# Performance work log

Measured on AMD Instinct MI355X. Metric: run time of the kernel, lower is better.

## Reference

```python
import jax, jax.numpy as jnp
import numpy as np

B, L, D = 2, 1024, 2048
E, K = 8, 2
H, HS = 1408, 2816


def setup_inputs() -> dict:
    key = jax.random.key(0)
    ks = jax.random.split(key, 9)
    s = 0.02  # param init scale
    return {
        "x": jax.random.normal(ks[0], (B, L, D), dtype=jnp.float32),
        "gate_w": jax.random.normal(ks[1], (E, D), dtype=jnp.float32) * s,
        "w_gate": jax.random.normal(ks[2], (E, D, H), dtype=jnp.float32) * s,
        "w_up": jax.random.normal(ks[3], (E, D, H), dtype=jnp.float32) * s,
        "w_down": jax.random.normal(ks[4], (E, H, D), dtype=jnp.float32) * s,
        "shgate_w": jax.random.normal(ks[5], (D,), dtype=jnp.float32) * s,
        "shw_gate": jax.random.normal(ks[6], (D, HS), dtype=jnp.float32) * s,
        "shw_up": jax.random.normal(ks[7], (D, HS), dtype=jnp.float32) * s,
        "shw_down": jax.random.normal(ks[8], (HS, D), dtype=jnp.float32) * s,
    }


def reference(x, gate_w, w_gate, w_up, w_down, shgate_w, shw_gate, shw_up, shw_down):
    b, l, d = x.shape
    xf = x.reshape(-1, d)  # [T, D]

    # --- router: softmax over expert logits, top-k, renormalize ---
    logits = jnp.einsum("td,ed->te", xf.astype(jnp.float32), gate_w)
    probs = jax.nn.softmax(logits.astype(jnp.float32), axis=-1)  # [T, E]
    weights, indices = jax.lax.top_k(probs, K)                   # [T, K]
    weights = (weights / weights.sum(-1, keepdims=True)).astype(x.dtype)

    # per-token combine weight for each expert: sum of top-k weights routed to e
    onehot = jax.nn.one_hot(indices, E, dtype=x.dtype)           # [T, K, E]
    combine = jnp.einsum("tk,tke->te", weights, onehot)          # [T, E]

    # --- experts (dense vectorized equivalent of masked gather/scatter loop) ---
    g = jnp.einsum("td,edh->teh", xf, w_gate)
    u = jnp.einsum("td,edh->teh", xf, w_up)
    h = jax.nn.silu(g) * u                                       # [T, E, H]
    # fused down-proj + weighted combine; accumulate in fp32 like the original
    out = jnp.einsum("teh,ehd,te->td", h.astype(jnp.float32),
                     w_down.astype(jnp.float32), combine.astype(jnp.float32))

    # --- shared expert with sigmoid gate ---
    sgate = jax.nn.sigmoid(xf @ shgate_w)[:, None]               # [T, 1]
    sh = (jax.nn.silu(xf @ shw_gate) * (xf @ shw_up)) @ shw_down  # [T, D]
    out = out + (sgate * sh).astype(jnp.float32)

    return out.astype(x.dtype).reshape(b, l, d)
```

## Files before the change

kernel.cpp:

```cpp
#include <hip/hip_runtime.h>
#include <hip/hip_bf16.h>
#include <math.h>

#define T_TOK 2048
#define Dd    2048
#define Ee    8
#define Hh    1408
#define HSs   2816
#define CAP   1024

typedef __attribute__((ext_vector_type(8))) __bf16 bf16x8;
typedef __attribute__((ext_vector_type(4))) __bf16 bf16x4;
typedef __attribute__((ext_vector_type(4))) float  f32x4;

#define MFMA(a, b, c) __builtin_amdgcn_mfma_f32_16x16x32_bf16(a, b, c, 0, 0, 0)

__device__ __forceinline__ void async_copy16(const __bf16* g, __bf16* l) {
    __builtin_amdgcn_global_load_lds(
        (const __attribute__((address_space(1))) unsigned int*)g,
        (__attribute__((address_space(3))) unsigned int*)l, 16, 0, 0);
}

__global__ void init_cnt(int* __restrict__ cnt) {
    if (threadIdx.x < Ee) cnt[threadIdx.x] = 0;
}

__global__ __launch_bounds__(256) void router_kernel(
    const float* __restrict__ x, const float* __restrict__ gate_w,
    const float* __restrict__ shgate_w,
    int* __restrict__ cnt, int* __restrict__ ptok,
    float* __restrict__ pw, float* __restrict__ sgate)
{
    const int t = blockIdx.x;
    const int tid = threadIdx.x;
    const float* xt = x + (size_t)t * Dd;

    float acc[Ee];
#pragma unroll
    for (int e = 0; e < Ee; e++) acc[e] = 0.f;
    float accs = 0.f;

    for (int d = tid; d < Dd; d += 256) {
        float xv = xt[d];
#pragma unroll
        for (int e = 0; e < Ee; e++) acc[e] += xv * gate_w[e * Dd + d];
        accs += xv * shgate_w[d];
    }

    __shared__ float red[Ee + 1][256];
#pragma unroll
    for (int e = 0; e < Ee; e++) red[e][tid] = acc[e];
    red[Ee][tid] = accs;
    __syncthreads();

    for (int s = 128; s > 0; s >>= 1) {
        if (tid < s) {
#pragma unroll
            for (int e = 0; e <= Ee; e++) red[e][tid] += red[e][tid + s];
        }
        __syncthreads();
    }

    if (tid == 0) {
        float l0 = -1e30f, l1 = -1e30f;
        int i0 = 0, i1 = 0;
#pragma unroll
        for (int e = 0; e < Ee; e++) {
            float v = red[e][0];
            if (v > l0) { l1 = l0; i1 = i0; l0 = v; i0 = e; }
            else if (v > l1) { l1 = v; i1 = e; }
        }
        float w0 = 1.f / (1.f + expf(l1 - l0));
        float w1 = 1.f - w0;

        int p0 = atomicAdd(&cnt[i0], 1);
        if (p0 < CAP) { ptok[i0 * CAP + p0] = t; pw[i0 * CAP + p0] = w0; }
        int p1 = atomicAdd(&cnt[i1], 1);
        if (p1 < CAP) { ptok[i1 * CAP + p1] = t; pw[i1 * CAP + p1] = w1; }

        sgate[t] = 1.f / (1.f + expf(-red[Ee][0]));
    }
}

__global__ __launch_bounds__(256) void cvt_x(const float* __restrict__ src,
                                             __bf16* __restrict__ dst)
{
    int i = blockIdx.x * 256 + threadIdx.x;
    float4 v = ((const float4*)src)[i];
    bf16x4 o = { (__bf16)v.x, (__bf16)v.y, (__bf16)v.z, (__bf16)v.w };
    ((bf16x4*)dst)[i] = o;
}

__global__ __launch_bounds__(256) void transpose_cvt(
    const float* __restrict__ src, __bf16* __restrict__ dst, int R, int C)
{
    const size_t bstride = (size_t)R * C;
    src += blockIdx.z * bstride;
    dst += blockIdx.z * bstride;
    __shared__ float tile[32][33];
    const int tx = threadIdx.x, ty = threadIdx.y;
    const int c0 = blockIdx.x * 32, r0 = blockIdx.y * 32;
#pragma unroll
    for (int j = 0; j < 4; j++)
        tile[ty + 8 * j][tx] = src[(size_t)(r0 + ty + 8 * j) * C + c0 + tx];
    __syncthreads();
#pragma unroll
    for (int j = 0; j < 4; j++)
        dst[(size_t)(c0 + ty + 8 * j) * R + r0 + tx] = (__bf16)tile[tx][ty + 8 * j];
}

__global__ __launch_bounds__(256, 3) void gateup_expert(
    const __bf16* __restrict__ xb,
    const __bf16* __restrict__ wgT, const __bf16* __restrict__ wuT,
    const int* __restrict__ cnt, const int* __restrict__ ptok,
    __bf16* __restrict__ hq)
{
    const int e = blockIdx.x >> 3, mt = blockIdx.x & 7;
    int n = cnt[e]; if (n > CAP) n = CAP;
    const int m0 = mt * 128;
    if (m0 >= n) return;
    const int h0 = blockIdx.y * 64;
    const int tid = threadIdx.x, lane = tid & 63, wave = tid >> 6;

    __shared__ __align__(16) __bf16 As[128 * 32];
    __shared__ __align__(16) __bf16 Bgs[64 * 32];
    __shared__ __align__(16) __bf16 Bus[64 * 32];
    __shared__ int tok_s[128];

    if (tid < 128) {
        int i = m0 + tid; int ic = i < n ? i : n - 1;
        tok_s[tid] = ptok[e * CAP + ic];
    }
    __syncthreads();

    const int kq = (tid & 3) * 8;
    const int r1 = tid >> 2, r2 = 64 + (tid >> 2);
    const __bf16* ga1 = xb + (size_t)tok_s[r1] * Dd + kq;
    const __bf16* ga2 = xb + (size_t)tok_s[r2] * Dd + kq;
    const size_t wbase = (size_t)e * Hh * Dd + (size_t)(h0 + (tid >> 2)) * Dd + kq;
    const __bf16* gbg = wgT + wbase;
    const __bf16* gbu = wuT + wbase;
    __bf16* la1 = As + tid * 8; __bf16* la2 = As + (tid + 256) * 8;
    __bf16* lbg = Bgs + tid * 8; __bf16* lbu = Bus + tid * 8;

    f32x4 accg[2][4] = {}, accu[2][4] = {};
    const int q = lane >> 4, m = lane & 15;

    for (int k0 = 0; k0 < Dd; k0 += 32) {
        async_copy16(ga1 + k0, la1);
        async_copy16(ga2 + k0, la2);
        async_copy16(gbg + k0, lbg);
        async_copy16(gbu + k0, lbu);
        __syncthreads();
        bf16x8 af[2], bgf[4], buf_[4];
        af[0] = *(const bf16x8*)(As + (wave * 32 + m) * 32 + q * 8);
        af[1] = *(const bf16x8*)(As + (wave * 32 + 16 + m) * 32 + q * 8);
#pragma unroll
        for (int j = 0; j < 4; j++) {
            bgf[j]  = *(const bf16x8*)(Bgs + (j * 16 + m) * 32 + q * 8);
            buf_[j] = *(const bf16x8*)(Bus + (j * 16 + m) * 32 + q * 8);
        }
#pragma unroll
        for (int i = 0; i < 2; i++)
#pragma unroll
            for (int j = 0; j < 4; j++) {
                accg[i][j] = MFMA(af[i], bgf[j], accg[i][j]);
                accu[i][j] = MFMA(af[i], buf_[j], accu[i][j]);
            }
        __syncthreads();
    }

#pragma unroll
    for (int i = 0; i < 2; i++)
#pragma unroll
        for (int r = 0; r < 4; r++) {
            int row = wave * 32 + i * 16 + q * 4 + r;
            size_t p = (size_t)(e * CAP + m0 + row);
#pragma unroll
            for (int j = 0; j < 4; j++) {
                int h = h0 + j * 16 + m;
                float g = accg[i][j][r], u = accu[i][j][r];
                float s = g / (1.f + __expf(-g));
                hq[p * Hh + h] = (__bf16)(s * u);
            }
        }
}

__global__ __launch_bounds__(256, 3) void gateup_shared(
    const __bf16* __restrict__ xb,
    const __bf16* __restrict__ wgT, const __bf16* __restrict__ wuT,
    __bf16* __restrict__ shh)
{
    const int m0 = blockIdx.x * 128;
    const int h0 = blockIdx.y * 64;
    const int tid = threadIdx.x, lane = tid & 63, wave = tid >> 6;

    __shared__ __align__(16) __bf16 As[128 * 32];
    __shared__ __align__(16) __bf16 Bgs[64 * 32];
    __shared__ __align__(16) __bf16 Bus[64 * 32];

    const int kq = (tid & 3) * 8;
    const __bf16* ga1 = xb + (size_t)(m0 + (tid >> 2)) * Dd + kq;
    const __bf16* ga2 = xb + (size_t)(m0 + 64 + (tid >> 2)) * Dd + kq;
    const size_t wbase = (size_t)(h0 + (tid >> 2)) * Dd + kq;
    const __bf16* gbg = wgT + wbase;
    const __bf16* gbu = wuT + wbase;
    __bf16* la1 = As + tid * 8; __bf16* la2 = As + (tid + 256) * 8;
    __bf16* lbg = Bgs + tid * 8; __bf16* lbu = Bus + tid * 8;

    f32x4 accg[2][4] = {}, accu[2][4] = {};
    const int q = lane >> 4, m = lane & 15;

    for (int k0 = 0; k0 < Dd; k0 += 32) {
        async_copy16(ga1 + k0, la1);
        async_copy16(ga2 + k0, la2);
        async_copy16(gbg + k0, lbg);
        async_copy16(gbu + k0, lbu);
        __syncthreads();
        bf16x8 af[2], bgf[4], buf_[4];
        af[0] = *(const bf16x8*)(As + (wave * 32 + m) * 32 + q * 8);
        af[1] = *(const bf16x8*)(As + (wave * 32 + 16 + m) * 32 + q * 8);
#pragma unroll
        for (int j = 0; j < 4; j++) {
            bgf[j]  = *(const bf16x8*)(Bgs + (j * 16 + m) * 32 + q * 8);
            buf_[j] = *(const bf16x8*)(Bus + (j * 16 + m) * 32 + q * 8);
        }
#pragma unroll
        for (int i = 0; i < 2; i++)
#pragma unroll
            for (int j = 0; j < 4; j++) {
                accg[i][j] = MFMA(af[i], bgf[j], accg[i][j]);
                accu[i][j] = MFMA(af[i], buf_[j], accu[i][j]);
            }
        __syncthreads();
    }

#pragma unroll
    for (int i = 0; i < 2; i++)
#pragma unroll
        for (int r = 0; r < 4; r++) {
            int row = wave * 32 + i * 16 + q * 4 + r;
#pragma unroll
            for (int j = 0; j < 4; j++) {
                int h = h0 + j * 16 + m;
                float g = accg[i][j][r], u = accu[i][j][r];
                float s = g / (1.f + __expf(-g));
                shh[(size_t)(m0 + row) * HSs + h] = (__bf16)(s * u);
            }
        }
}

__global__ __launch_bounds__(256, 3) void down_shared(
    const __bf16* __restrict__ A,
    const __bf16* __restrict__ BT,
    const float* __restrict__ sgate,
    float* __restrict__ out)
{
    const int m0 = blockIdx.x * 128, n0 = blockIdx.y * 128;
    const int tid = threadIdx.x, lane = tid & 63, wave = tid >> 6;
    const int wr = wave >> 1, wc = wave & 1;

    __shared__ __align__(16) __bf16 As[128 * 32];
    __shared__ __align__(16) __bf16 Bs[128 * 32];

    const int kq = (tid & 3) * 8;
    const __bf16* ga1 = A + (size_t)(m0 + (tid >> 2)) * HSs + kq;
    const __bf16* ga2 = A + (size_t)(m0 + 64 + (tid >> 2)) * HSs + kq;
    const __bf16* gb1 = BT + (size_t)(n0 + (tid >> 2)) * HSs + kq;
    const __bf16* gb2 = BT + (size_t)(n0 + 64 + (tid >> 2)) * HSs + kq;
    __bf16* la1 = As + tid * 8; __bf16* la2 = As + (tid + 256) * 8;
    __bf16* lb1 = Bs + tid * 8; __bf16* lb2 = Bs + (tid + 256) * 8;

    f32x4 acc[4][4] = {};
    const int q = lane >> 4, m = lane & 15;

    for (int k0 = 0; k0 < HSs; k0 += 32) {
        async_copy16(ga1 + k0, la1);
        async_copy16(ga2 + k0, la2);
        async_copy16(gb1 + k0, lb1);
        async_copy16(gb2 + k0, lb2);
        __syncthreads();
        bf16x8 af[4], bf[4];
#pragma unroll
        for (int i = 0; i < 4; i++) {
            af[i] = *(const bf16x8*)(As + (wr * 64 + i * 16 + m) * 32 + q * 8);
            bf[i] = *(const bf16x8*)(Bs + (wc * 64 + i * 16 + m) * 32 + q * 8);
        }
#pragma unroll
        for (int i = 0; i < 4; i++)
#pragma unroll
            for (int j = 0; j < 4; j++)
                acc[i][j] = MFMA(af[i], bf[j], acc[i][j]);
        __syncthreads();
    }

#pragma unroll
    for (int i = 0; i < 4; i++)
#pragma unroll
        for (int r = 0; r < 4; r++) {
            int t = m0 + wr * 64 + i * 16 + q * 4 + r;
            float sg = sgate[t];
#pragma unroll
            for (int j = 0; j < 4; j++) {
                int d = n0 + wc * 64 + j * 16 + m;
                out[(size_t)t * Dd + d] = sg * acc[i][j][r];
            }
        }
}

__global__ __launch_bounds__(256, 3) void down_expert(
    const __bf16* __restrict__ hq,
    const __bf16* __restrict__ wdT,
    const int* __restrict__ cnt, const int* __restrict__ ptok,
    const float* __restrict__ pw,
    float* __restrict__ out)
{
    const int e = blockIdx.x >> 3, mt = blockIdx.x & 7;
    int n = cnt[e]; if (n > CAP) n = CAP;
    const int m0 = mt * 128;
    if (m0 >= n) return;
    const int n0 = blockIdx.y * 128;
    const int tid = threadIdx.x, lane = tid & 63, wave = tid >> 6;
    const int wr = wave >> 1, wc = wave & 1;

    __shared__ __align__(16) __bf16 As[128 * 32];
    __shared__ __align__(16) __bf16 Bs[128 * 32];
    __shared__ int   tok_s[128];
    __shared__ float w_s[128];

    if (tid < 128) {
        int i = m0 + tid; int ic = i < n ? i : n - 1;
        tok_s[tid] = ptok[e * CAP + ic];
        w_s[tid] = (i < n) ? pw[e * CAP + ic] : 0.f;
    }

    const int kq = (tid & 3) * 8;
    int i1 = m0 + (tid >> 2);       if (i1 > n - 1) i1 = n - 1;
    int i2 = m0 + 64 + (tid >> 2);  if (i2 > n - 1) i2 = n - 1;
    const __bf16* ga1 = hq + (size_t)(e * CAP + i1) * Hh + kq;
    const __bf16* ga2 = hq + (size_t)(e * CAP + i2) * Hh + kq;
    const __bf16* gb1 = wdT + ((size_t)e * Dd + n0 + (tid >> 2)) * Hh + kq;
    const __bf16* gb2 = wdT + ((size_t)e * Dd + n0 + 64 + (tid >> 2)) * Hh + kq;
    __bf16* la1 = As + tid * 8; __bf16* la2 = As + (tid + 256) * 8;
    __bf16* lb1 = Bs + tid * 8; __bf16* lb2 = Bs + (tid + 256) * 8;

    f32x4 acc[4][4] = {};
    const int q = lane >> 4, m = lane & 15;

    for (int k0 = 0; k0 < Hh; k0 += 32) {
        async_copy16(ga1 + k0, la1);
        async_copy16(ga2 + k0, la2);
        async_copy16(gb1 + k0, lb1);
        async_copy16(gb2 + k0, lb2);
        __syncthreads();
        bf16x8 af[4], bf[4];
#pragma unroll
        for (int i = 0; i < 4; i++) {
            af[i] = *(const bf16x8*)(As + (wr * 64 + i * 16 + m) * 32 + q * 8);
            bf[i] = *(const bf16x8*)(Bs + (wc * 64 + i * 16 + m) * 32 + q * 8);
        }
#pragma unroll
        for (int i = 0; i < 4; i++)
#pragma unroll
            for (int j = 0; j < 4; j++)
                acc[i][j] = MFMA(af[i], bf[j], acc[i][j]);
        __syncthreads();
    }

#pragma unroll
    for (int i = 0; i < 4; i++)
#pragma unroll
        for (int r = 0; r < 4; r++) {
            int row = wr * 64 + i * 16 + q * 4 + r;
            if (m0 + row < n) {
                int   tok = tok_s[row];
                float w   = w_s[row];
#pragma unroll
                for (int j = 0; j < 4; j++) {
                    int d = n0 + wc * 64 + j * 16 + m;
                    atomicAdd(&out[(size_t)tok * Dd + d], w * acc[i][j][r]);
                }
            }
        }
}

extern "C" void kernel_launch(void* const* d_in, const int* in_sizes, int n_in,
                              void* d_out, int out_size, void* d_ws, size_t ws_size,
                              hipStream_t stream) {
    const float* x        = (const float*)d_in[0];
    const float* gate_w   = (const float*)d_in[1];
    const float* w_gate   = (const float*)d_in[2];
    const float* w_up     = (const float*)d_in[3];
    const float* w_down   = (const float*)d_in[4];
    const float* shgate_w = (const float*)d_in[5];
    const float* shw_gate = (const float*)d_in[6];
    const float* shw_up   = (const float*)d_in[7];
    const float* shw_down = (const float*)d_in[8];
    float* out = (float*)d_out;

    char* ws = (char*)d_ws;
    size_t off = 0;
    auto alloc = [&](size_t bytes) { char* p = ws + off; off = (off + bytes + 255) & ~(size_t)255; return p; };
    int*    cnt    = (int*)   alloc(Ee * 4);
    int*    ptok   = (int*)   alloc(Ee * CAP * 4);
    float*  pw     = (float*) alloc(Ee * CAP * 4);
    float*  sgate  = (float*) alloc(T_TOK * 4);
    __bf16* xb     = (__bf16*)alloc((size_t)T_TOK * Dd * 2);
    __bf16* wgT    = (__bf16*)alloc((size_t)Ee * Hh * Dd * 2);
    __bf16* wuT    = (__bf16*)alloc((size_t)Ee * Hh * Dd * 2);
    __bf16* wdT    = (__bf16*)alloc((size_t)Ee * Dd * Hh * 2);
    __bf16* shwgT  = (__bf16*)alloc((size_t)HSs * Dd * 2);
    __bf16* shwuT  = (__bf16*)alloc((size_t)HSs * Dd * 2);
    __bf16* shwdT  = (__bf16*)alloc((size_t)Dd * HSs * 2);
    __bf16* hq     = (__bf16*)alloc((size_t)Ee * CAP * Hh * 2);
    __bf16* shh    = (__bf16*)alloc((size_t)T_TOK * HSs * 2);

    dim3 b256(256), bT(32, 8);

    init_cnt<<<dim3(1), dim3(64), 0, stream>>>(cnt);
    cvt_x<<<dim3(T_TOK * Dd / 4 / 256), b256, 0, stream>>>(x, xb);
    transpose_cvt<<<dim3(Hh / 32, Dd / 32, Ee), bT, 0, stream>>>(w_gate, wgT, Dd, Hh);
    transpose_cvt<<<dim3(Hh / 32, Dd / 32, Ee), bT, 0, stream>>>(w_up, wuT, Dd, Hh);
    transpose_cvt<<<dim3(Dd / 32, Hh / 32, Ee), bT, 0, stream>>>(w_down, wdT, Hh, Dd);
    transpose_cvt<<<dim3(HSs / 32, Dd / 32, 1), bT, 0, stream>>>(shw_gate, shwgT, Dd, HSs);
    transpose_cvt<<<dim3(HSs / 32, Dd / 32, 1), bT, 0, stream>>>(shw_up, shwuT, Dd, HSs);
    transpose_cvt<<<dim3(Dd / 32, HSs / 32, 1), bT, 0, stream>>>(shw_down, shwdT, HSs, Dd);

    router_kernel<<<dim3(T_TOK), b256, 0, stream>>>(x, gate_w, shgate_w, cnt, ptok, pw, sgate);

    gateup_expert<<<dim3(Ee * 8, Hh / 64), b256, 0, stream>>>(xb, wgT, wuT, cnt, ptok, hq);
    gateup_shared<<<dim3(T_TOK / 128, HSs / 64), b256, 0, stream>>>(xb, shwgT, shwuT, shh);
    down_shared<<<dim3(T_TOK / 128, Dd / 128), b256, 0, stream>>>(shh, shwdT, sgate, out);
    down_expert<<<dim3(Ee * 8, Dd / 128), b256, 0, stream>>>(hq, wdT, cnt, ptok, pw, out);
}
```

Baseline: 763.2 us.

## Merge expert and shared GEMMs into single launches, replace atomics with slot combine

Expert and shared-expert gate/up GEMMs now run in one kernel, and both down-projection GEMMs run in another. This cuts launches and lets the two workloads fill the GPU together. Expert outputs go to a per-token slot buffer instead of float atomicAdd into the output, and a separate combine kernel sums the slots. The LDS staging is laid out per-wave to match the MFMA fragment layout, and the weight transpose uses 64x64 tiles with paired bf16 stores. The cost is an extra 32MB fp32 intermediate plus a combine pass over it. Gate/up tiles are also split across waves, exchanging the up accumulators through LDS.

```diff
diff --git a/kernel.cpp b/kernel.cpp
--- a/kernel.cpp
+++ b/kernel.cpp
@@ -11,6 +11,7 @@
 
 typedef __attribute__((ext_vector_type(8))) __bf16 bf16x8;
 typedef __attribute__((ext_vector_type(4))) __bf16 bf16x4;
+typedef __attribute__((ext_vector_type(2))) __bf16 bf16x2;
 typedef __attribute__((ext_vector_type(4))) float  f32x4;
 
 #define MFMA(a, b, c) __builtin_amdgcn_mfma_f32_16x16x32_bf16(a, b, c, 0, 0, 0)
@@ -28,7 +29,7 @@
 __global__ __launch_bounds__(256) void router_kernel(
     const float* __restrict__ x, const float* __restrict__ gate_w,
     const float* __restrict__ shgate_w,
-    int* __restrict__ cnt, int* __restrict__ ptok,
+    int* __restrict__ cnt, int* __restrict__ ptok, int* __restrict__ pslot,
     float* __restrict__ pw, float* __restrict__ sgate)
 {
     const int t = blockIdx.x;
@@ -74,10 +75,15 @@
         float w1 = 1.f - w0;
 
         int p0 = atomicAdd(&cnt[i0], 1);
-        if (p0 < CAP) { ptok[i0 * CAP + p0] = t; pw[i0 * CAP + p0] = w0; }
+        if (p0 < CAP) {
+            ptok[i0 * CAP + p0] = t; pslot[i0 * CAP + p0] = 2 * t;
+            pw[i0 * CAP + p0] = w0;
+        }
         int p1 = atomicAdd(&cnt[i1], 1);
-        if (p1 < CAP) { ptok[i1 * CAP + p1] = t; pw[i1 * CAP + p1] = w1; }
-
+        if (p1 < CAP) {
+            ptok[i1 * CAP + p1] = t; pslot[i1 * CAP + p1] = 2 * t + 1;
+            pw[i1 * CAP + p1] = w1;
+        }
         sgate[t] = 1.f / (1.f + expf(-red[Ee][0]));
     }
 }
@@ -94,276 +100,208 @@
 __global__ __launch_bounds__(256) void transpose_cvt(
     const float* __restrict__ src, __bf16* __restrict__ dst, int R, int C)
 {
-    const size_t bstride = (size_t)R * C;
-    src += blockIdx.z * bstride;
-    dst += blockIdx.z * bstride;
-    __shared__ float tile[32][33];
-    const int tx = threadIdx.x, ty = threadIdx.y;
-    const int c0 = blockIdx.x * 32, r0 = blockIdx.y * 32;
-#pragma unroll
-    for (int j = 0; j < 4; j++)
-        tile[ty + 8 * j][tx] = src[(size_t)(r0 + ty + 8 * j) * C + c0 + tx];
+    src += (size_t)blockIdx.z * R * C;
+    dst += (size_t)blockIdx.z * R * C;
+    __shared__ float tile[64][65];
+    const int tid = threadIdx.x, tx = tid & 63, ty = tid >> 6;
+    const int c0 = blockIdx.x * 64, r0 = blockIdx.y * 64;
+#pragma unroll
+    for (int j = 0; j < 16; j++) {
+        int r = j * 4 + ty;
+        tile[r][tx] = src[(size_t)(r0 + r) * C + c0 + tx];
+    }
     __syncthreads();
-#pragma unroll
-    for (int j = 0; j < 4; j++)
-        dst[(size_t)(c0 + ty + 8 * j) * R + r0 + tx] = (__bf16)tile[tx][ty + 8 * j];
-}
-
-__global__ __launch_bounds__(256, 3) void gateup_expert(
+    const int rp = (tid & 31) * 2;
+    const int cg = tid >> 5;
+#pragma unroll
+    for (int j = 0; j < 8; j++) {
+        int c = j * 8 + cg;
+        bf16x2 v = { (__bf16)tile[rp][c], (__bf16)tile[rp + 1][c] };
+        *(bf16x2*)&dst[(size_t)(c0 + c) * R + r0 + rp] = v;
+    }
+}
+
+__global__ __launch_bounds__(256, 3) void gateup_all(
     const __bf16* __restrict__ xb,
     const __bf16* __restrict__ wgT, const __bf16* __restrict__ wuT,
+    const __bf16* __restrict__ shwgT, const __bf16* __restrict__ shwuT,
     const int* __restrict__ cnt, const int* __restrict__ ptok,
-    __bf16* __restrict__ hq)
-{
-    const int e = blockIdx.x >> 3, mt = blockIdx.x & 7;
-    int n = cnt[e]; if (n > CAP) n = CAP;
-    const int m0 = mt * 128;
-    if (m0 >= n) return;
-    const int h0 = blockIdx.y * 64;
-    const int tid = threadIdx.x, lane = tid & 63, wave = tid >> 6;
-
-    __shared__ __align__(16) __bf16 As[128 * 32];
-    __shared__ __align__(16) __bf16 Bgs[64 * 32];
-    __shared__ __align__(16) __bf16 Bus[64 * 32];
-    __shared__ int tok_s[128];
-
-    if (tid < 128) {
-        int i = m0 + tid; int ic = i < n ? i : n - 1;
-        tok_s[tid] = ptok[e * CAP + ic];
-    }
-    __syncthreads();
-
-    const int kq = (tid & 3) * 8;
-    const int r1 = tid >> 2, r2 = 64 + (tid >> 2);
-    const __bf16* ga1 = xb + (size_t)tok_s[r1] * Dd + kq;
-    const __bf16* ga2 = xb + (size_t)tok_s[r2] * Dd + kq;
-    const size_t wbase = (size_t)e * Hh * Dd + (size_t)(h0 + (tid >> 2)) * Dd + kq;
-    const __bf16* gbg = wgT + wbase;
-    const __bf16* gbu = wuT + wbase;
-    __bf16* la1 = As + tid * 8; __bf16* la2 = As + (tid + 256) * 8;
-    __bf16* lbg = Bgs + tid * 8; __bf16* lbu = Bus + tid * 8;
-
-    f32x4 accg[2][4] = {}, accu[2][4] = {};
-    const int q = lane >> 4, m = lane & 15;
-
-    for (int k0 = 0; k0 < Dd; k0 += 32) {
-        async_copy16(ga1 + k0, la1);
-        async_copy16(ga2 + k0, la2);
-        async_copy16(gbg + k0, lbg);
-        async_copy16(gbu + k0, lbu);
-        __syncthreads();
-        bf16x8 af[2], bgf[4], buf_[4];
-        af[0] = *(const bf16x8*)(As + (wave * 32 + m) * 32 + q * 8);
-        af[1] = *(const bf16x8*)(As + (wave * 32 + 16 + m) * 32 + q * 8);
-#pragma unroll
-        for (int j = 0; j < 4; j++) {
-            bgf[j]  = *(const bf16x8*)(Bgs + (j * 16 + m) * 32 + q * 8);
-            buf_[j] = *(const bf16x8*)(Bus + (j * 16 + m) * 32 + q * 8);
-        }
-#pragma unroll
-        for (int i = 0; i < 2; i++)
-#pragma unroll
-            for (int j = 0; j < 4; j++) {
-                accg[i][j] = MFMA(af[i], bgf[j], accg[i][j]);
-                accu[i][j] = MFMA(af[i], buf_[j], accu[i][j]);
-            }
-        __syncthreads();
-    }
-
-#pragma unroll
-    for (int i = 0; i < 2; i++)
-#pragma unroll
-        for (int r = 0; r < 4; r++) {
-            int row = wave * 32 + i * 16 + q * 4 + r;
-            size_t p = (size_t)(e * CAP + m0 + row);
-#pragma unroll
-            for (int j = 0; j < 4; j++) {
-                int h = h0 + j * 16 + m;
-                float g = accg[i][j][r], u = accu[i][j][r];
-                float s = g / (1.f + __expf(-g));
-                hq[p * Hh + h] = (__bf16)(s * u);
-            }
-        }
-}
-
-__global__ __launch_bounds__(256, 3) void gateup_shared(
-    const __bf16* __restrict__ xb,
-    const __bf16* __restrict__ wgT, const __bf16* __restrict__ wuT,
-    __bf16* __restrict__ shh)
-{
-    const int m0 = blockIdx.x * 128;
-    const int h0 = blockIdx.y * 64;
-    const int tid = threadIdx.x, lane = tid & 63, wave = tid >> 6;
-
-    __shared__ __align__(16) __bf16 As[128 * 32];
-    __shared__ __align__(16) __bf16 Bgs[64 * 32];
-    __shared__ __align__(16) __bf16 Bus[64 * 32];
-
-    const int kq = (tid & 3) * 8;
-    const __bf16* ga1 = xb + (size_t)(m0 + (tid >> 2)) * Dd + kq;
-    const __bf16* ga2 = xb + (size_t)(m0 + 64 + (tid >> 2)) * Dd + kq;
-    const size_t wbase = (size_t)(h0 + (tid >> 2)) * Dd + kq;
-    const __bf16* gbg = wgT + wbase;
-    const __bf16* gbu = wuT + wbase;
-    __bf16* la1 = As + tid * 8; __bf16* la2 = As + (tid + 256) * 8;
-    __bf16* lbg = Bgs + tid * 8; __bf16* lbu = Bus + tid * 8;
-
-    f32x4 accg[2][4] = {}, accu[2][4] = {};
-    const int q = lane >> 4, m = lane & 15;
-
-    for (int k0 = 0; k0 < Dd; k0 += 32) {
-        async_copy16(ga1 + k0, la1);
-        async_copy16(ga2 + k0, la2);
-        async_copy16(gbg + k0, lbg);
-        async_copy16(gbu + k0, lbu);
-        __syncthreads();
-        bf16x8 af[2], bgf[4], buf_[4];
-        af[0] = *(const bf16x8*)(As + (wave * 32 + m) * 32 + q * 8);
-        af[1] = *(const bf16x8*)(As + (wave * 32 + 16 + m) * 32 + q * 8);
-#pragma unroll
-        for (int j = 0; j < 4; j++) {
-            bgf[j]  = *(const bf16x8*)(Bgs + (j * 16 + m) * 32 + q * 8);
-            buf_[j] = *(const bf16x8*)(Bus + (j * 16 + m) * 32 + q * 8);
-        }
-#pragma unroll
-        for (int i = 0; i < 2; i++)
-#pragma unroll
-            for (int j = 0; j < 4; j++) {
-                accg[i][j] = MFMA(af[i], bgf[j], accg[i][j]);
-                accu[i][j] = MFMA(af[i], buf_[j], accu[i][j]);
-            }
-        __syncthreads();
-    }
-
-#pragma unroll
-    for (int i = 0; i < 2; i++)
-#pragma unroll
-        for (int r = 0; r < 4; r++) {
-            int row = wave * 32 + i * 16 + q * 4 + r;
-#pragma unroll
-            for (int j = 0; j < 4; j++) {
-                int h = h0 + j * 16 + m;
-                float g = accg[i][j][r], u = accu[i][j][r];
-                float s = g / (1.f + __expf(-g));
-                shh[(size_t)(m0 + row) * HSs + h] = (__bf16)(s * u);
-            }
-        }
-}
-
-__global__ __launch_bounds__(256, 3) void down_shared(
-    const __bf16* __restrict__ A,
-    const __bf16* __restrict__ BT,
-    const float* __restrict__ sgate,
-    float* __restrict__ out)
-{
-    const int m0 = blockIdx.x * 128, n0 = blockIdx.y * 128;
+    __bf16* __restrict__ hq, __bf16* __restrict__ shh)
+{
+    const int bx = blockIdx.x;
     const int tid = threadIdx.x, lane = tid & 63, wave = tid >> 6;
     const int wr = wave >> 1, wc = wave & 1;
-
-    __shared__ __align__(16) __bf16 As[128 * 32];
-    __shared__ __align__(16) __bf16 Bs[128 * 32];
-
-    const int kq = (tid & 3) * 8;
-    const __bf16* ga1 = A + (size_t)(m0 + (tid >> 2)) * HSs + kq;
-    const __bf16* ga2 = A + (size_t)(m0 + 64 + (tid >> 2)) * HSs + kq;
-    const __bf16* gb1 = BT + (size_t)(n0 + (tid >> 2)) * HSs + kq;
-    const __bf16* gb2 = BT + (size_t)(n0 + 64 + (tid >> 2)) * HSs + kq;
-    __bf16* la1 = As + tid * 8; __bf16* la2 = As + (tid + 256) * 8;
-    __bf16* lb1 = Bs + tid * 8; __bf16* lb2 = Bs + (tid + 256) * 8;
+    const int lm = lane & 15, lq = lane >> 4;
+
+    bool sh;
+    int m0, h0, n, e = 0;
+    const __bf16 *bg_mat, *bu_mat;
+    if (bx < 1408) {
+        sh = false;
+        int mtg = bx / 22, ht = bx - mtg * 22;
+        e = mtg >> 3; m0 = (mtg & 7) * 128; h0 = ht * 64;
+        n = cnt[e]; if (n > CAP) n = CAP;
+        if (m0 >= n) return;
+        bg_mat = wgT + (size_t)e * Hh * Dd;
+        bu_mat = wuT + (size_t)e * Hh * Dd;
+    } else {
+        sh = true;
+        int s = bx - 1408;
+        int mt = s / 44, ht = s - mt * 44;
+        m0 = mt * 128; h0 = ht * 64; n = T_TOK;
+        bg_mat = shwgT; bu_mat = shwuT;
+    }
+
+    __shared__ __align__(16) __bf16 stage[8192];
+    __shared__ int tok_s[128];
+
+    if (tid < 128) {
+        int i = m0 + tid;
+        if (sh) tok_s[tid] = i;
+        else { int ic = i < n ? i : n - 1; tok_s[tid] = ptok[e * CAP + ic]; }
+    }
+    __syncthreads();
+
+    const __bf16* pa0 = xb + (size_t)tok_s[wave * 16 + lm] * Dd + lq * 8;
+    const __bf16* pa1 = xb + (size_t)tok_s[64 + wave * 16 + lm] * Dd + lq * 8;
+    const __bf16* pbg = bg_mat + (size_t)(h0 + wave * 16 + lm) * Dd + lq * 8;
+    const __bf16* pbu = bu_mat + (size_t)(h0 + wave * 16 + lm) * Dd + lq * 8;
+    __bf16* la0 = stage + wave * 512 + lane * 8;
+    __bf16* la1 = stage + (4 + wave) * 512 + lane * 8;
+    __bf16* lbg = stage + 4096 + wave * 512 + lane * 8;
+    __bf16* lbu = stage + 6144 + wave * 512 + lane * 8;
 
     f32x4 acc[4][4] = {};
-    const int q = lane >> 4, m = lane & 15;
-
-    for (int k0 = 0; k0 < HSs; k0 += 32) {
-        async_copy16(ga1 + k0, la1);
-        async_copy16(ga2 + k0, la2);
-        async_copy16(gb1 + k0, lb1);
-        async_copy16(gb2 + k0, lb2);
-        __syncthreads();
-        bf16x8 af[4], bf[4];
-#pragma unroll
-        for (int i = 0; i < 4; i++) {
-            af[i] = *(const bf16x8*)(As + (wr * 64 + i * 16 + m) * 32 + q * 8);
-            bf[i] = *(const bf16x8*)(Bs + (wc * 64 + i * 16 + m) * 32 + q * 8);
-        }
+
+    for (int k0 = 0; k0 < Dd; k0 += 32) {
+        async_copy16(pa0, la0); async_copy16(pa1, la1);
+        async_copy16(pbg, lbg); async_copy16(pbu, lbu);
+        pa0 += 32; pa1 += 32; pbg += 32; pbu += 32;
+        __syncthreads();
+        bf16x8 af[4], bfr[4];
+        const __bf16* bbase = stage + (wc ? 6144 : 4096);
+#pragma unroll
+        for (int i = 0; i < 4; i++)
+            af[i] = *(const bf16x8*)(stage + (wr * 4 + i) * 512 + lane * 8);
+#pragma unroll
+        for (int j = 0; j < 4; j++)
+            bfr[j] = *(const bf16x8*)(bbase + j * 512 + lane * 8);
 #pragma unroll
         for (int i = 0; i < 4; i++)
 #pragma unroll
             for (int j = 0; j < 4; j++)
-                acc[i][j] = MFMA(af[i], bf[j], acc[i][j]);
-        __syncthreads();
-    }
-
-#pragma unroll
-    for (int i = 0; i < 4; i++)
-#pragma unroll
-        for (int r = 0; r < 4; r++) {
-            int t = m0 + wr * 64 + i * 16 + q * 4 + r;
-            float sg = sgate[t];
+                acc[i][j] = MFMA(af[i], bfr[j], acc[i][j]);
+        __syncthreads();
+    }
+
+    if (wc == 1) {
+#pragma unroll
+        for (int i = 0; i < 4; i++)
 #pragma unroll
             for (int j = 0; j < 4; j++) {
-                int d = n0 + wc * 64 + j * 16 + m;
-                out[(size_t)t * Dd + d] = sg * acc[i][j][r];
+                bf16x4 uv;
+#pragma unroll
+                for (int r = 0; r < 4; r++) uv[r] = (__bf16)acc[i][j][r];
+                *(bf16x4*)(stage + ((wr * 4 + i) * 4 + j) * 256 + lane * 4) = uv;
             }
-        }
-}
-
-__global__ __launch_bounds__(256, 3) void down_expert(
-    const __bf16* __restrict__ hq,
-    const __bf16* __restrict__ wdT,
-    const int* __restrict__ cnt, const int* __restrict__ ptok,
-    const float* __restrict__ pw,
-    float* __restrict__ out)
-{
-    const int e = blockIdx.x >> 3, mt = blockIdx.x & 7;
-    int n = cnt[e]; if (n > CAP) n = CAP;
-    const int m0 = mt * 128;
-    if (m0 >= n) return;
-    const int n0 = blockIdx.y * 128;
+    }
+    __syncthreads();
+    if (wc == 0) {
+#pragma unroll
+        for (int i = 0; i < 4; i++)
+#pragma unroll
+            for (int j = 0; j < 4; j++) {
+                bf16x4 uv = *(const bf16x4*)(stage + ((wr * 4 + i) * 4 + j) * 256 + lane * 4);
+                int col = h0 + j * 16 + lm;
+#pragma unroll
+                for (int r = 0; r < 4; r++) {
+                    int grow = m0 + wr * 64 + i * 16 + lq * 4 + r;
+                    if (!sh && grow >= n) continue;
+                    float g = acc[i][j][r], u = (float)uv[r];
+                    float hv = g / (1.f + __expf(-g)) * u;
+                    if (sh) shh[(size_t)grow * HSs + col] = (__bf16)hv;
+                    else    hq[((size_t)e * CAP + grow) * Hh + col] = (__bf16)hv;
+                }
+            }
+    }
+}
+
+__global__ __launch_bounds__(256, 3) void down_all(
+    const __bf16* __restrict__ hq, const __bf16* __restrict__ wdT,
+    const __bf16* __restrict__ shh, const __bf16* __restrict__ shwdT,
+    const int* __restrict__ cnt, const int* __restrict__ pslot,
+    const float* __restrict__ pw, const float* __restrict__ sgate,
+    float* __restrict__ eo, float* __restrict__ out)
+{
+    const int bx = blockIdx.x;
     const int tid = threadIdx.x, lane = tid & 63, wave = tid >> 6;
     const int wr = wave >> 1, wc = wave & 1;
-
-    __shared__ __align__(16) __bf16 As[128 * 32];
-    __shared__ __align__(16) __bf16 Bs[128 * 32];
-    __shared__ int   tok_s[128];
+    const int lm = lane & 15, lq = lane >> 4;
+
+    bool sh;
+    int m0, n0, n, e = 0, kdim;
+    if (bx < 1024) {
+        sh = false;
+        e = bx >> 7; m0 = ((bx >> 4) & 7) * 128; n0 = (bx & 15) * 128;
+        n = cnt[e]; if (n > CAP) n = CAP;
+        if (m0 >= n) return;
+        kdim = Hh;
+    } else {
+        sh = true;
+        int s = bx - 1024;
+        m0 = (s >> 4) * 128; n0 = (s & 15) * 128; n = T_TOK;
+        kdim = HSs;
+    }
+
+    __shared__ __align__(16) __bf16 stage[8192];
+    __shared__ int   slot_s[128];
     __shared__ float w_s[128];
 
-    if (tid < 128) {
+    if (!sh && tid < 128) {
         int i = m0 + tid; int ic = i < n ? i : n - 1;
-        tok_s[tid] = ptok[e * CAP + ic];
+        slot_s[tid] = pslot[e * CAP + ic];
         w_s[tid] = (i < n) ? pw[e * CAP + ic] : 0.f;
     }
 
-    const int kq = (tid & 3) * 8;
-    int i1 = m0 + (tid >> 2);       if (i1 > n - 1) i1 = n - 1;
-    int i2 = m0 + 64 + (tid >> 2);  if (i2 > n - 1) i2 = n - 1;
-    const __bf16* ga1 = hq + (size_t)(e * CAP + i1) * Hh + kq;
-    const __bf16* ga2 = hq + (size_t)(e * CAP + i2) * Hh + kq;
-    const __bf16* gb1 = wdT + ((size_t)e * Dd + n0 + (tid >> 2)) * Hh + kq;
-    const __bf16* gb2 = wdT + ((size_t)e * Dd + n0 + 64 + (tid >> 2)) * Hh + kq;
-    __bf16* la1 = As + tid * 8; __bf16* la2 = As + (tid + 256) * 8;
-    __bf16* lb1 = Bs + tid * 8; __bf16* lb2 = Bs + (tid + 256) * 8;
+    int ar0 = m0 + wave * 16 + lm, ar1 = m0 + 64 + wave * 16 + lm;
+    const __bf16 *pa0, *pa1, *pb0, *pb1;
+    if (sh) {
+        pa0 = shh + (size_t)ar0 * HSs + lq * 8;
+        pa1 = shh + (size_t)ar1 * HSs + lq * 8;
+        pb0 = shwdT + (size_t)(n0 + wave * 16 + lm) * HSs + lq * 8;
+        pb1 = shwdT + (size_t)(n0 + 64 + wave * 16 + lm) * HSs + lq * 8;
+    } else {
+        int a0c = ar0 < n ? ar0 : n - 1;
+        int a1c = ar1 < n ? ar1 : n - 1;
+        pa0 = hq + ((size_t)e * CAP + a0c) * Hh + lq * 8;
+        pa1 = hq + ((size_t)e * CAP + a1c) * Hh + lq * 8;
+        pb0 = wdT + ((size_t)e * Dd + n0 + wave * 16 + lm) * Hh + lq * 8;
+        pb1 = wdT + ((size_t)e * Dd + n0 + 64 + wave * 16 + lm) * Hh + lq * 8;
+    }
+    __bf16* la0 = stage + wave * 512 + lane * 8;
+    __bf16* la1 = stage + (4 + wave) * 512 + lane * 8;
+    __bf16* lb0 = stage + 4096 + wave * 512 + lane * 8;
+    __bf16* lb1 = stage + 4096 + (4 + wave) * 512 + lane * 8;
 
     f32x4 acc[4][4] = {};
-    const int q = lane >> 4, m = lane & 15;
-
-    for (int k0 = 0; k0 < Hh; k0 += 32) {
-        async_copy16(ga1 + k0, la1);
-        async_copy16(ga2 + k0, la2);
-        async_copy16(gb1 + k0, lb1);
-        async_copy16(gb2 + k0, lb2);
-        __syncthreads();
-        bf16x8 af[4], bf[4];
-#pragma unroll
-        for (int i = 0; i < 4; i++) {
-            af[i] = *(const bf16x8*)(As + (wr * 64 + i * 16 + m) * 32 + q * 8);
-            bf[i] = *(const bf16x8*)(Bs + (wc * 64 + i * 16 + m) * 32 + q * 8);
-        }
+
+    for (int k0 = 0; k0 < kdim; k0 += 32) {
+        async_copy16(pa0, la0); async_copy16(pa1, la1);
+        async_copy16(pb0, lb0); async_copy16(pb1, lb1);
+        pa0 += 32; pa1 += 32; pb0 += 32; pb1 += 32;
+        __syncthreads();
+        bf16x8 af[4], bfr[4];
+#pragma unroll
+        for (int i = 0; i < 4; i++)
+            af[i] = *(const bf16x8*)(stage + (wr * 4 + i) * 512 + lane * 8);
+#pragma unroll
+        for (int j = 0; j < 4; j++)
+            bfr[j] = *(const bf16x8*)(stage + 4096 + (wc * 4 + j) * 512 + lane * 8);
 #pragma unroll
         for (int i = 0; i < 4; i++)
 #pragma unroll
             for (int j = 0; j < 4; j++)
-                acc[i][j] = MFMA(af[i], bf[j], acc[i][j]);
+                acc[i][j] = MFMA(af[i], bfr[j], acc[i][j]);
         __syncthreads();
     }
 
@@ -371,17 +309,34 @@
     for (int i = 0; i < 4; i++)
 #pragma unroll
         for (int r = 0; r < 4; r++) {
-            int row = wr * 64 + i * 16 + q * 4 + r;
-            if (m0 + row < n) {
-                int   tok = tok_s[row];
-                float w   = w_s[row];
-#pragma unroll
-                for (int j = 0; j < 4; j++) {
-                    int d = n0 + wc * 64 + j * 16 + m;
-                    atomicAdd(&out[(size_t)tok * Dd + d], w * acc[i][j][r]);
-                }
+            int rloc = wr * 64 + i * 16 + lq * 4 + r;
+            if (sh) {
+                int t = m0 + rloc;
+                float sg = sgate[t];
+#pragma unroll
+                for (int j = 0; j < 4; j++)
+                    out[(size_t)t * Dd + n0 + (wc * 4 + j) * 16 + lm] = sg * acc[i][j][r];
+            } else if (m0 + rloc < n) {
+                int   slot = slot_s[rloc];
+                float w    = w_s[rloc];
+#pragma unroll
+                for (int j = 0; j < 4; j++)
+                    eo[(size_t)slot * Dd + n0 + (wc * 4 + j) * 16 + lm] = w * acc[i][j][r];
             }
         }
+}
+
+__global__ __launch_bounds__(256) void combine_kernel(
+    const float* __restrict__ eo, float* __restrict__ out)
+{
+    int i4 = blockIdx.x * 256 + threadIdx.x;
+    int t = i4 >> 9;
+    int c = i4 & 511;
+    float4 o = ((const float4*)out)[i4];
+    float4 a = ((const float4*)(eo + (size_t)(2 * t) * Dd))[c];
+    float4 b = ((const float4*)(eo + (size_t)(2 * t + 1) * Dd))[c];
+    o.x += a.x + b.x; o.y += a.y + b.y; o.z += a.z + b.z; o.w += a.w + b.w;
+    ((float4*)out)[i4] = o;
 }
 
 extern "C" void kernel_launch(void* const* d_in, const int* in_sizes, int n_in,
@@ -403,6 +358,7 @@
     auto alloc = [&](size_t bytes) { char* p = ws + off; off = (off + bytes + 255) & ~(size_t)255; return p; };
     int*    cnt    = (int*)   alloc(Ee * 4);
     int*    ptok   = (int*)   alloc(Ee * CAP * 4);
+    int*    pslot  = (int*)   alloc(Ee * CAP * 4);
     float*  pw     = (float*) alloc(Ee * CAP * 4);
     float*  sgate  = (float*) alloc(T_TOK * 4);
     __bf16* xb     = (__bf16*)alloc((size_t)T_TOK * Dd * 2);
@@ -414,22 +370,24 @@
     __bf16* shwdT  = (__bf16*)alloc((size_t)Dd * HSs * 2);
     __bf16* hq     = (__bf16*)alloc((size_t)Ee * CAP * Hh * 2);
     __bf16* shh    = (__bf16*)alloc((size_t)T_TOK * HSs * 2);
-
-    dim3 b256(256), bT(32, 8);
+    float*  eo     = (float*) alloc((size_t)T_TOK * 2 * Dd * 4);
+
+    dim3 b256(256);
 
     init_cnt<<<dim3(1), dim3(64), 0, stream>>>(cnt);
+    router_kernel<<<dim3(T_TOK), b256, 0, stream>>>(
+        x, gate_w, shgate_w, cnt, ptok, pslot, pw, sgate);
     cvt_x<<<dim3(T_TOK * Dd / 4 / 256), b256, 0, stream>>>(x, xb);
-    transpose_cvt<<<dim3(Hh / 32, Dd / 32, Ee), bT, 0, stream>>>(w_gate, wgT, Dd, Hh);
-    transpose_cvt<<<dim3(Hh / 32, Dd / 32, Ee), bT, 0, stream>>>(w_up, wuT, Dd, Hh);
-    transpose_cvt<<<dim3(Dd / 32, Hh / 32, Ee), bT, 0, stream>>>(w_down, wdT, Hh, Dd);
-    transpose_cvt<<<dim3(HSs / 32, Dd / 32, 1), bT, 0, stream>>>(shw_gate, shwgT, Dd, HSs);
-    transpose_cvt<<<dim3(HSs / 32, Dd / 32, 1), bT, 0, stream>>>(shw_up, shwuT, Dd, HSs);
-    transpose_cvt<<<dim3(Dd / 32, HSs / 32, 1), bT, 0, stream>>>(shw_down, shwdT, HSs, Dd);
-
-    router_kernel<<<dim3(T_TOK), b256, 0, stream>>>(x, gate_w, shgate_w, cnt, ptok, pw, sgate);
-
-    gateup_expert<<<dim3(Ee * 8, Hh / 64), b256, 0, stream>>>(xb, wgT, wuT, cnt, ptok, hq);
-    gateup_shared<<<dim3(T_TOK / 128, HSs / 64), b256, 0, stream>>>(xb, shwgT, shwuT, shh);
-    down_shared<<<dim3(T_TOK / 128, Dd / 128), b256, 0, stream>>>(shh, shwdT, sgate, out);
-    down_expert<<<dim3(Ee * 8, Dd / 128), b256, 0, stream>>>(hq, wdT, cnt, ptok, pw, out);
-}
+    transpose_cvt<<<dim3(Hh / 64, Dd / 64, Ee), b256, 0, stream>>>(w_gate, wgT, Dd, Hh);
+    transpose_cvt<<<dim3(Hh / 64, Dd / 64, Ee), b256, 0, stream>>>(w_up, wuT, Dd, Hh);
+    transpose_cvt<<<dim3(Dd / 64, Hh / 64, Ee), b256, 0, stream>>>(w_down, wdT, Hh, Dd);
+    transpose_cvt<<<dim3(HSs / 64, Dd / 64, 1), b256, 0, stream>>>(shw_gate, shwgT, Dd, HSs);
+    transpose_cvt<<<dim3(HSs / 64, Dd / 64, 1), b256, 0, stream>>>(shw_up, shwuT, Dd, HSs);
+    transpose_cvt<<<dim3(Dd / 64, HSs / 64, 1), b256, 0, stream>>>(shw_down, shwdT, HSs, Dd);
+
+    gateup_all<<<dim3(1408 + 704), b256, 0, stream>>>(
+        xb, wgT, wuT, shwgT, shwuT, cnt, ptok, hq, shh);
+    down_all<<<dim3(1024 + 256), b256, 0, stream>>>(
+        hq, wdT, shh, shwdT, cnt, pslot, pw, sgate, eo, out);
+    combine_kernel<<<dim3(T_TOK * Dd / 4 / 256), b256, 0, stream>>>(eo, out);
+}
```

Result: slower. 811.7 us (+6.4%).
